# Kernel optimization log

Hardware: AMD Instinct MI355X
Metric: run time of the kernel (lower is better)

## Reference

```python
import jax, jax.numpy as jnp
import numpy as np

B = 8
A = 1614
TOPN = 6
IOU_THR = 0.25
PAD = 224
OUT = 224

def _make_anchors():
    # 6 anchor shapes on the 14x14 map, 6 on 7x7, 9 on 4x4 -> 1614 total,
    # ordered anchor-type-major then row-major spatial to match the [C,H,W] flatten
    # of the tidy conv outputs (as generate_default_anchor_maps does in NTS-Net).
    specs = [
        (14, 32.0, [(48, 48), (64, 48), (48, 64), (80, 80), (96, 64), (64, 96)]),
        (7, 64.0, [(96, 96), (128, 96), (96, 128), (160, 160), (192, 128), (128, 192)]),
        (4, 112.0, [(192, 192), (256, 192), (192, 256), (288, 288), (320, 256), (256, 320), (352, 352), (384, 320), (320, 384)]),
    ]
    blocks = []
    for fm, stride, sizes in specs:
        c = (np.arange(fm) + 0.5) * stride
        cy, cx = np.meshgrid(c, c, indexing='ij')
        for (h, w) in sizes:
            blocks.append(np.stack([cy - h / 2, cx - w / 2, cy + h / 2, cx + w / 2], -1).reshape(-1, 4))
    a = (np.concatenate(blocks, 0) + PAD).astype(np.int64)  # mimic (edge_anchors+224).astype(int)
    return a.astype(np.float32)  # [1614,4] (y0,x0,y1,x1) in padded-image coords

def _conv(x, w, b, stride, pad):
    y = jax.lax.conv_general_dilated(x, w, (stride, stride), [(pad, pad), (pad, pad)],
                                     dimension_numbers=('NCHW', 'OIHW', 'NCHW'))
    return y + b[None, :, None, None]

def _rpn_scores(rpn, wd1, bd1, wd2, bd2, wd3, bd3, wt1, bt1, wt2, bt2, wt3, bt3):
    b = rpn.shape[0]
    d1 = jax.nn.relu(_conv(rpn, wd1, bd1, 1, 1))   # [B,128,14,14]
    d2 = jax.nn.relu(_conv(d1, wd2, bd2, 2, 1))    # [B,128,7,7]
    d3 = jax.nn.relu(_conv(d2, wd3, bd3, 2, 1))    # [B,128,4,4]
    t1 = _conv(d1, wt1, bt1, 1, 0).reshape(b, -1)  # [B,1176]
    t2 = _conv(d2, wt2, bt2, 1, 0).reshape(b, -1)  # [B,294]
    t3 = _conv(d3, wt3, bt3, 1, 0).reshape(b, -1)  # [B,144]
    return jnp.concatenate([t1, t2, t3], axis=1)   # [B,1614]

def _nms_keep(boxes, scores):
    # Greedy NMS over all A anchors; returns keep mask in ORIGINAL anchor order.
    order = jnp.argsort(-scores)
    b = boxes[order]
    y0, x0, y1, x1 = b[:, 0], b[:, 1], b[:, 2], b[:, 3]
    area = (y1 - y0) * (x1 - x0)
    ih = jnp.clip(jnp.minimum(y1[:, None], y1[None, :]) - jnp.maximum(y0[:, None], y0[None, :]), 0)
    iw = jnp.clip(jnp.minimum(x1[:, None], x1[None, :]) - jnp.maximum(x0[:, None], x0[None, :]), 0)
    inter = ih * iw
    iou = inter / (area[:, None] + area[None, :] - inter)
    idx = jnp.arange(A)
    def body(i, supp):
        row = (iou[i] > IOU_THR) & (idx > i)
        return jnp.where(supp[i], supp, supp | row)
    supp = jax.lax.fori_loop(0, A, body, jnp.zeros((A,), bool))
    return jnp.zeros((A,), bool).at[order].set(~supp)

def _crop_resize(img, box):
    # img [3,Hp,Wp]; box int32 (x0,y0,x1,y1).
    # Equivalent to F.interpolate(img[:, y0:y1, x0:x1], (224,224), 'bilinear', align_corners=True)
    x0, y0, x1, y1 = box[0], box[1], box[2], box[3]
    t = jnp.arange(OUT, dtype=jnp.float32) / (OUT - 1)
    sy = y0.astype(jnp.float32) + t * (y1 - 1 - y0).astype(jnp.float32)
    sx = x0.astype(jnp.float32) + t * (x1 - 1 - x0).astype(jnp.float32)
    y0i = jnp.floor(sy).astype(jnp.int32); x0i = jnp.floor(sx).astype(jnp.int32)
    y1i = jnp.minimum(y0i + 1, y1 - 1);    x1i = jnp.minimum(x0i + 1, x1 - 1)
    wy = (sy - y0i.astype(jnp.float32))[None, :, None]
    wx = (sx - x0i.astype(jnp.float32))[None, None, :]
    g = lambda yi, xi: img[:, yi][:, :, xi]  # gather rows then cols -> [3,224,224]
    top = (1 - wx) * g(y0i, x0i) + wx * g(y0i, x1i)
    bot = (1 - wx) * g(y1i, x0i) + wx * g(y1i, x1i)
    return (1 - wy) * top + wy * bot

def setup_inputs():
    key = jax.random.key(0)
    ks = jax.random.split(key, 16)
    n = jax.random.normal
    return {
        'x': n(ks[0], (B, 3, 448, 448), jnp.float32),
        'rpn_feature': n(ks[1], (B, 2048, 14, 14), jnp.float32),
        'anchors': jnp.asarray(_make_anchors()),
        'wd1': 0.02 * n(ks[2], (128, 2048, 3, 3), jnp.float32), 'bd1': 0.01 * n(ks[3], (128,), jnp.float32),
        'wd2': 0.05 * n(ks[4], (128, 128, 3, 3), jnp.float32),  'bd2': 0.01 * n(ks[5], (128,), jnp.float32),
        'wd3': 0.05 * n(ks[6], (128, 128, 3, 3), jnp.float32),  'bd3': 0.01 * n(ks[7], (128,), jnp.float32),
        'wt1': 0.1 * n(ks[8], (6, 128, 1, 1), jnp.float32),     'bt1': 0.01 * n(ks[9], (6,), jnp.float32),
        'wt2': 0.1 * n(ks[10], (6, 128, 1, 1), jnp.float32),    'bt2': 0.01 * n(ks[11], (6,), jnp.float32),
        'wt3': 0.1 * n(ks[12], (9, 128, 1, 1), jnp.float32),    'bt3': 0.01 * n(ks[13], (9,), jnp.float32),
    }

def reference(x, rpn_feature, anchors, wd1, bd1, wd2, bd2, wd3, bd3, wt1, bt1, wt2, bt2, wt3, bt3):
    scores = _rpn_scores(rpn_feature, wd1, bd1, wd2, bd2, wd3, bd3, wt1, bt1, wt2, bt2, wt3, bt3)
    keep = jax.vmap(lambda s: _nms_keep(anchors, s))(scores)           # [B,A] bool
    masked = jnp.where(keep, scores, -jnp.inf)
    top_prob, top_idx = jax.lax.top_k(masked, TOPN)                    # [B,6]
    tb = anchors[top_idx]                                              # [B,6,4] (y0,x0,y1,x1)
    coords = jnp.stack([tb[..., 1], tb[..., 0], tb[..., 3], tb[..., 2]], -1)  # (x0,y0,x1,y1)
    x_pad = jnp.pad(x, ((0, 0), (0, 0), (PAD, PAD), (PAD, PAD)))       # [B,3,896,896]
    bint = coords.astype(jnp.int32)
    part_imgs = jax.vmap(lambda img, bs: jax.vmap(lambda bb: _crop_resize(img, bb))(bs))(x_pad, bint)  # [B,6,3,224,224]
    return part_imgs, coords, top_prob, top_idx
```

## Files before the change

kernel.cpp:

```cpp
#include <hip/hip_runtime.h>
#include <hip/hip_bf16.h>
#include <math.h>
#include <stdint.h>


#define OFF_COORDS 7225344
#define OFF_PROB   7225536
#define OFF_IDX    7225584
#define NA 1614
#define K1TOT 18432

typedef __attribute__((ext_vector_type(8)))  short  short8;
typedef __attribute__((ext_vector_type(16))) float  floatx16;

__global__ __launch_bounds__(256) void k_prep_all(
    const float* __restrict__ rpn,
    const float* __restrict__ wd1,
    const float* __restrict__ wd2,
    const float* __restrict__ wd3,
    __hip_bfloat16* __restrict__ ah,  __hip_bfloat16* __restrict__ al,
    __hip_bfloat16* __restrict__ b1h, __hip_bfloat16* __restrict__ b1l,
    __hip_bfloat16* __restrict__ b2h, __hip_bfloat16* __restrict__ b2l,
    __hip_bfloat16* __restrict__ b3h, __hip_bfloat16* __restrict__ b3l)
{
    const int bid = blockIdx.x;
    const int t   = threadIdx.x;
    if (bid < 1024) {
        __shared__ float tile[64][65];
        const int cib  = (bid & 31) * 64;
        const int posb = ((bid >> 5) & 3) * 64;
        const int b    = bid >> 7;
#pragma unroll
        for (int it = 0; it < 16; ++it) {
            int idx  = it * 256 + t;
            int cil  = idx >> 6;
            int posl = idx & 63;
            int pos  = posb + posl;
            int py = pos >> 4, px = pos & 15;
            int y = py - 1, x = px - 1;
            float v = 0.0f;
            if ((unsigned)y < 14u && (unsigned)x < 14u)
                v = rpn[((size_t)(b * 2048 + cib + cil) * 14 + y) * 14 + x];
            tile[cil][posl] = v;
        }
        __syncthreads();
#pragma unroll
        for (int it = 0; it < 16; ++it) {
            int idx  = it * 256 + t;
            int posl = idx >> 6;
            int cil  = idx & 63;
            float v = tile[cil][posl];
            __hip_bfloat16 h = __float2bfloat16(v);
            __hip_bfloat16 l = __float2bfloat16(v - __bfloat162float(h));
            size_t o = (size_t)(b * 256 + posb + posl) * 2048 + cib + cil;
            ah[o] = h; al[o] = l;
        }
    } else if (bid < 2176) {
        int local = bid - 1024;
        int tap = local % 9;
        int co  = local / 9;
#pragma unroll
        for (int i = 0; i < 8; ++i) {
            int ci = i * 256 + t;
            float v = wd1[((size_t)co * 2048 + ci) * 9 + tap];
            __hip_bfloat16 h = __float2bfloat16(v);
            __hip_bfloat16 l = __float2bfloat16(v - __bfloat162float(h));
            size_t o = (size_t)co * K1TOT + tap * 2048 + ci;
            b1h[o] = h; b1l[o] = l;
        }
    } else {
        int local = bid - 2176;
        int z  = local >= 576;
        int l3 = z ? (local - 576) : local;
        int tap = l3 % 9;
        int co  = (l3 / 9) * 2 + (t >> 7);
        int ci  = t & 127;
        const float* w = z ? wd3 : wd2;
        __hip_bfloat16* bh = z ? b3h : b2h;
        __hip_bfloat16* bl = z ? b3l : b2l;
        float v = w[((size_t)co * 128 + ci) * 9 + tap];
        __hip_bfloat16 h = __float2bfloat16(v);
        __hip_bfloat16 l = __float2bfloat16(v - __bfloat162float(h));
        size_t o = (size_t)co * 1152 + tap * 128 + ci;
        bh[o] = h; bl[o] = l;
    }
}

template<int POSN, int OW, int STR, int CIN, int MTOT, bool SWIZ>
__global__ __launch_bounds__(256) void k_conv_mfma(const short* __restrict__ ah,
                                                   const short* __restrict__ al,
                                                   const short* __restrict__ bh,
                                                   const short* __restrict__ bl,
                                                   float* __restrict__ partial,
                                                   int chunk, int kpx, int mtiles)
{
    constexpr int KTOT = CIN * 9;
    __shared__ short AsH[128][40];
    __shared__ short AsL[128][40];
    __shared__ short BsH[128][40];
    __shared__ short BsL[128][40];

    int mt, kc;
    if (SWIZ) {
        int bid = blockIdx.x;
        int xcd = bid & 7;
        int idx = bid >> 3;
        int q   = idx / mtiles;
        kc = xcd * kpx + q;
        mt = idx - q * mtiles;
    } else {
        mt = blockIdx.x;
        kc = blockIdx.y;
    }

    const int t     = threadIdx.x;
    const int lane  = t & 63;
    const int w     = t >> 6;
    const int wm    = (w & 1) * 64;
    const int wn    = (w >> 1) * 64;
    const int lm    = lane & 31;
    const int half  = lane >> 5;
    const int mbase = mt * 128;
    const int k0    = kc * chunk;
    const int k1    = (k0 + chunk < KTOT) ? (k0 + chunk) : KTOT;

    int arow[2], apos[2]; bool aval[2];
    const int akc = (t & 3) * 8;
#pragma unroll
    for (int i = 0; i < 2; ++i) {
        int row = ((i * 256 + t) >> 2);
        int m   = mbase + row;
        arow[i] = row;
        aval[i] = (m < MTOT);
        int mm = aval[i] ? m : 0;
        int b  = mm / POSN;
        int p  = mm - b * POSN;
        int y  = p / OW;
        int x  = p - y * OW;
        apos[i] = b * 256 + y * STR * 16 + x * STR;
    }

    floatx16 acc[2][2];
#pragma unroll
    for (int mf = 0; mf < 2; ++mf)
#pragma unroll
        for (int nf = 0; nf < 2; ++nf)
#pragma unroll
            for (int r = 0; r < 16; ++r) acc[mf][nf][r] = 0.0f;

    const short8 zero8 = {0, 0, 0, 0, 0, 0, 0, 0};

    for (int ks = k0; ks < k1; ks += 32) {
        const int tap = ks / CIN;
        const int ci0 = ks - tap * CIN;
        const int dy  = tap / 3, dx = tap - dy * 3;
#pragma unroll
        for (int i = 0; i < 2; ++i) {
            short8 vh = zero8, vl = zero8;
            if (aval[i]) {
                size_t g = (size_t)(apos[i] + dy * 16 + dx) * CIN + ci0 + akc;
                vh = *(const short8*)(ah + g);
                vl = *(const short8*)(al + g);
            }
            *(short8*)&AsH[arow[i]][akc] = vh;
            *(short8*)&AsL[arow[i]][akc] = vl;
        }
#pragma unroll
        for (int i = 0; i < 2; ++i) {
            int n = ((i * 256 + t) >> 2);
            size_t g = (size_t)n * KTOT + ks + akc;
            *(short8*)&BsH[n][akc] = *(const short8*)(bh + g);
            *(short8*)&BsL[n][akc] = *(const short8*)(bl + g);
        }
        __syncthreads();
#pragma unroll
        for (int kst = 0; kst < 2; ++kst) {
            const int koff = kst * 16 + half * 8;
            short8 a_h[2], a_l[2], b_h[2], b_l[2];
#pragma unroll
            for (int mf = 0; mf < 2; ++mf) {
                a_h[mf] = *(const short8*)&AsH[wm + mf * 32 + lm][koff];
                a_l[mf] = *(const short8*)&AsL[wm + mf * 32 + lm][koff];
            }
#pragma unroll
            for (int nf = 0; nf < 2; ++nf) {
                b_h[nf] = *(const short8*)&BsH[wn + nf * 32 + lm][koff];
                b_l[nf] = *(const short8*)&BsL[wn + nf * 32 + lm][koff];
            }
#pragma unroll
            for (int mf = 0; mf < 2; ++mf)
#pragma unroll
                for (int nf = 0; nf < 2; ++nf) {
                    acc[mf][nf] = __builtin_amdgcn_mfma_f32_32x32x16_bf16(
                        a_h[mf], b_h[nf], acc[mf][nf], 0, 0, 0);
                    acc[mf][nf] = __builtin_amdgcn_mfma_f32_32x32x16_bf16(
                        a_h[mf], b_l[nf], acc[mf][nf], 0, 0, 0);
                    acc[mf][nf] = __builtin_amdgcn_mfma_f32_32x32x16_bf16(
                        a_l[mf], b_h[nf], acc[mf][nf], 0, 0, 0);
                }
        }
        __syncthreads();
    }

    float* P = partial + (size_t)kc * MTOT * 128;
#pragma unroll
    for (int mf = 0; mf < 2; ++mf)
#pragma unroll
        for (int nf = 0; nf < 2; ++nf)
#pragma unroll
            for (int r = 0; r < 16; ++r) {
                int row = (r & 3) + 8 * (r >> 2) + 4 * half;
                int m = mbase + wm + mf * 32 + row;
                int n = wn + nf * 32 + lm;
                if (m < MTOT) P[(size_t)m * 128 + n] = acc[mf][nf][r];
            }
}

template<int POSN, int OWV>
__global__ __launch_bounds__(256) void k_reduce_pad(const float* __restrict__ partial,
                                                    const float* __restrict__ bias,
                                                    float* __restrict__ dn,
                                                    __hip_bfloat16* __restrict__ ph,
                                                    __hip_bfloat16* __restrict__ pl,
                                                    int S)
{
    constexpr int MTOT = 8 * POSN;
    int idx = blockIdx.x * 256 + threadIdx.x;
    int b   = idx >> 15;
    int pos = (idx >> 7) & 255;
    int co  = idx & 127;
    int y = (pos >> 4) - 1;
    int x = (pos & 15) - 1;
    if ((unsigned)y < (unsigned)OWV && (unsigned)x < (unsigned)OWV) {
        int m = b * POSN + y * OWV + x;
        float s = bias[co];
        for (int k = 0; k < S; ++k) s += partial[(size_t)k * MTOT * 128 + m * 128 + co];
        s = fmaxf(s, 0.0f);
        dn[(size_t)m * 128 + co] = s;
        __hip_bfloat16 h = __float2bfloat16(s);
        __hip_bfloat16 l = __float2bfloat16(s - __bfloat162float(h));
        ph[idx] = h; pl[idx] = l;
    } else {
        ph[idx] = __float2bfloat16(0.0f);
        pl[idx] = __float2bfloat16(0.0f);
    }
}

__global__ __launch_bounds__(256) void k_reduce3(const float* __restrict__ partial,
                                                 const float* __restrict__ bias,
                                                 float* __restrict__ dn, int S)
{
    int idx = blockIdx.x * 256 + threadIdx.x;
    int co  = idx & 127;
    float s = bias[co];
    for (int k = 0; k < S; ++k) s += partial[(size_t)k * 128 * 128 + idx];
    dn[idx] = fmaxf(s, 0.0f);
}

__global__ __launch_bounds__(256) void k_heads(const float* __restrict__ d1n,
                                               const float* __restrict__ d2n,
                                               const float* __restrict__ d3n,
                                               const float* __restrict__ w1, const float* __restrict__ b1,
                                               const float* __restrict__ w2, const float* __restrict__ b2,
                                               const float* __restrict__ w3, const float* __restrict__ b3,
                                               float* __restrict__ scores)
{
    int idx = blockIdx.x * 256 + threadIdx.x;
    if (idx >= 8 * NA) return;
    int b = idx / NA;
    int e = idx - b * NA;
    const float* d; const float* w; float bias;
    if (e < 1176) {
        int c = e / 196, p = e - c * 196;
        d = d1n + (size_t)(b * 196 + p) * 128; w = w1 + c * 128; bias = b1[c];
    } else if (e < 1470) {
        int e2 = e - 1176; int c = e2 / 49, p = e2 - c * 49;
        d = d2n + (size_t)(b * 49 + p) * 128; w = w2 + c * 128; bias = b2[c];
    } else {
        int e2 = e - 1470; int c = e2 / 16, p = e2 - c * 16;
        d = d3n + (size_t)(b * 16 + p) * 128; w = w3 + c * 128; bias = b3[c];
    }
    float s = bias;
#pragma unroll
    for (int i = 0; i < 32; ++i) {
        float4 dv = ((const float4*)d)[i];
        float4 wv = ((const float4*)w)[i];
        s = fmaf(dv.x, wv.x, s);
        s = fmaf(dv.y, wv.y, s);
        s = fmaf(dv.z, wv.z, s);
        s = fmaf(dv.w, wv.w, s);
    }
    scores[idx] = s;
}

__global__ __launch_bounds__(256) void k_nms_topk(const float* __restrict__ scores,
                                                  const float* __restrict__ anchors,
                                                  float* __restrict__ out,
                                                  int* __restrict__ boxes)
{
    __shared__ float ms[NA];
    __shared__ float ay0[NA], ax0[NA], ay1[NA], ax1[NA];
    __shared__ unsigned char picked[NA];
    __shared__ float rv[4]; __shared__ int ri[4];
    __shared__ float win[5];
    int b = blockIdx.x;
    int t = threadIdx.x;
    for (int i = t; i < NA; i += 256) {
        ms[i] = scores[b * NA + i];
        float4 an = ((const float4*)anchors)[i];
        ay0[i] = an.x; ax0[i] = an.y; ay1[i] = an.z; ax1[i] = an.w;
        picked[i] = 0;
    }
    __syncthreads();
    for (int r = 0; r < 6; ++r) {
        float bv = -INFINITY; int bi = NA;
        for (int i = t; i < NA; i += 256) {
            if (!picked[i]) {
                float v = ms[i];
                if (v > bv || (v == bv && i < bi)) { bv = v; bi = i; }
            }
        }
#pragma unroll
        for (int off = 32; off > 0; off >>= 1) {
            float v2 = __shfl_down(bv, off);
            int   i2 = __shfl_down(bi, off);
            if (v2 > bv || (v2 == bv && i2 < bi)) { bv = v2; bi = i2; }
        }
        if ((t & 63) == 0) { rv[t >> 6] = bv; ri[t >> 6] = bi; }
        __syncthreads();
        if (t == 0) {
            bv = rv[0]; bi = ri[0];
            for (int wv = 1; wv < 4; ++wv)
                if (rv[wv] > bv || (rv[wv] == bv && ri[wv] < bi)) { bv = rv[wv]; bi = ri[wv]; }
            picked[bi] = 1;
            win[0] = ay0[bi]; win[1] = ax0[bi]; win[2] = ay1[bi]; win[3] = ax1[bi]; win[4] = bv;
            int o = b * 6 + r;
            out[OFF_COORDS + o * 4 + 0] = ax0[bi];
            out[OFF_COORDS + o * 4 + 1] = ay0[bi];
            out[OFF_COORDS + o * 4 + 2] = ax1[bi];
            out[OFF_COORDS + o * 4 + 3] = ay1[bi];
            out[OFF_PROB + o] = bv;
            out[OFF_IDX  + o] = (float)bi;
            boxes[o * 4 + 0] = (int)ax0[bi];
            boxes[o * 4 + 1] = (int)ay0[bi];
            boxes[o * 4 + 2] = (int)ax1[bi];
            boxes[o * 4 + 3] = (int)ay1[bi];
        }
        __syncthreads();
        float by0 = win[0], bx0 = win[1], by1 = win[2], bx1 = win[3];
        float barea = (by1 - by0) * (bx1 - bx0);
        for (int i = t; i < NA; i += 256) {
            if (picked[i]) continue;
            float ih = fmaxf(fminf(by1, ay1[i]) - fmaxf(by0, ay0[i]), 0.0f);
            float iw = fmaxf(fminf(bx1, ax1[i]) - fmaxf(bx0, ax0[i]), 0.0f);
            float inter = ih * iw;
            float area  = (ay1[i] - ay0[i]) * (ax1[i] - ax0[i]);
            float iou = inter / (barea + area - inter);
            if (iou > 0.25f) ms[i] = -INFINITY;
        }
        __syncthreads();
    }
}

__global__ __launch_bounds__(256) void k_crop(const float* __restrict__ x,
                                              const int* __restrict__ boxes,
                                              float* __restrict__ out)
{
    int lin = blockIdx.x * 256 + threadIdx.x;
    int i    = lin % 224;
    int rest = lin / 224;
    int j    = rest % 224;
    int rc   = rest / 224;
    int c    = rc % 3;
    int br   = rc / 3;
    int b    = br / 6;
    int4 bx = ((const int4*)boxes)[br];
    float tj = (float)j / 223.0f;
    float sy = (float)bx.y + tj * (float)(bx.w - 1 - bx.y);
    int y0i = (int)floorf(sy);
    int y1i = min(y0i + 1, bx.w - 1);
    float wy = sy - (float)y0i;
    float ti = (float)i / 223.0f;
    float sx = (float)bx.x + ti * (float)(bx.z - 1 - bx.x);
    int x0i = (int)floorf(sx);
    int x1i = min(x0i + 1, bx.z - 1);
    float wx = sx - (float)x0i;
    const float* img = x + ((size_t)b * 3 + c) * 448 * 448;
    auto g = [&](int yy, int xx) -> float {
        yy -= 224; xx -= 224;
        if ((unsigned)yy >= 448u || (unsigned)xx >= 448u) return 0.0f;
        return img[(size_t)yy * 448 + xx];
    };
    float g00 = g(y0i, x0i), g01 = g(y0i, x1i);
    float g10 = g(y1i, x0i), g11 = g(y1i, x1i);
    float top = (1.0f - wx) * g00 + wx * g01;
    float bot = (1.0f - wx) * g10 + wx * g11;
    out[lin] = (1.0f - wy) * top + wy * bot;
}

extern "C" void kernel_launch(void* const* d_in, const int* in_sizes, int n_in,
                              void* d_out, int out_size, void* d_ws, size_t ws_size,
                              hipStream_t stream)
{
    (void)in_sizes; (void)n_in; (void)out_size;
    const float* x    = (const float*)d_in[0];
    const float* rpn  = (const float*)d_in[1];
    const float* anch = (const float*)d_in[2];
    const float* wd1  = (const float*)d_in[3];
    const float* bd1  = (const float*)d_in[4];
    const float* wd2  = (const float*)d_in[5];
    const float* bd2  = (const float*)d_in[6];
    const float* wd3  = (const float*)d_in[7];
    const float* bd3  = (const float*)d_in[8];
    const float* hw1  = (const float*)d_in[9];
    const float* hb1  = (const float*)d_in[10];
    const float* hw2  = (const float*)d_in[11];
    const float* hb2  = (const float*)d_in[12];
    const float* hw3  = (const float*)d_in[13];
    const float* hb3  = (const float*)d_in[14];
    float* out = (float*)d_out;

    char* ws = (char*)d_ws;
    size_t off = 0;
    auto alloc = [&](size_t bytes) -> void* {
        void* p = ws + off;
        off = (off + bytes + 255) & ~(size_t)255;
        return p;
    };
    __hip_bfloat16* ahb  = (__hip_bfloat16*)alloc((size_t)8 * 256 * 2048 * 2);
    __hip_bfloat16* alb  = (__hip_bfloat16*)alloc((size_t)8 * 256 * 2048 * 2);
    __hip_bfloat16* b1h  = (__hip_bfloat16*)alloc((size_t)128 * K1TOT * 2);
    __hip_bfloat16* b1l  = (__hip_bfloat16*)alloc((size_t)128 * K1TOT * 2);
    __hip_bfloat16* b2h  = (__hip_bfloat16*)alloc((size_t)128 * 1152 * 2);
    __hip_bfloat16* b2l  = (__hip_bfloat16*)alloc((size_t)128 * 1152 * 2);
    __hip_bfloat16* b3h  = (__hip_bfloat16*)alloc((size_t)128 * 1152 * 2);
    __hip_bfloat16* b3l  = (__hip_bfloat16*)alloc((size_t)128 * 1152 * 2);
    __hip_bfloat16* d1ph = (__hip_bfloat16*)alloc((size_t)8 * 256 * 128 * 2);
    __hip_bfloat16* d1pl = (__hip_bfloat16*)alloc((size_t)8 * 256 * 128 * 2);
    __hip_bfloat16* d2ph = (__hip_bfloat16*)alloc((size_t)8 * 256 * 128 * 2);
    __hip_bfloat16* d2pl = (__hip_bfloat16*)alloc((size_t)8 * 256 * 128 * 2);
    float* d1n  = (float*)alloc((size_t)8 * 196 * 128 * 4);
    float* d2n  = (float*)alloc((size_t)8 * 49 * 128 * 4);
    float* d3n  = (float*)alloc((size_t)8 * 16 * 128 * 4);
    float* sc   = (float*)alloc((size_t)8 * NA * 4);
    int*  boxes = (int*)alloc((size_t)8 * 6 * 4 * 4);
    size_t avail = (ws_size > off) ? (ws_size - off) : 0;
    float* P = (float*)(ws + off);

    int S1 = (avail >= (size_t)64 * 1568 * 128 * 4) ? 64 : 48;
    if (avail < (size_t)48 * 1568 * 128 * 4) S1 = 32;
    int chunk1 = K1TOT / S1;
    int kpx1   = S1 / 8;

    k_prep_all<<<dim3(3328), 256, 0, stream>>>(rpn, wd1, wd2, wd3,
        ahb, alb, b1h, b1l, b2h, b2l, b3h, b3l);

    k_conv_mfma<196, 14, 1, 2048, 1568, true><<<dim3(13 * S1), 256, 0, stream>>>(
        (const short*)ahb, (const short*)alb, (const short*)b1h, (const short*)b1l,
        P, chunk1, kpx1, 13);
    k_reduce_pad<196, 14><<<dim3(1024), 256, 0, stream>>>(P, bd1, d1n, d1ph, d1pl, S1);

    k_conv_mfma<49, 7, 2, 128, 392, false><<<dim3(4, 9), 256, 0, stream>>>(
        (const short*)d1ph, (const short*)d1pl, (const short*)b2h, (const short*)b2l,
        P, 128, 0, 0);
    k_reduce_pad<49, 7><<<dim3(1024), 256, 0, stream>>>(P, bd2, d2n, d2ph, d2pl, 9);

    k_conv_mfma<16, 4, 2, 128, 128, false><<<dim3(1, 9), 256, 0, stream>>>(
        (const short*)d2ph, (const short*)d2pl, (const short*)b3h, (const short*)b3l,
        P, 128, 0, 0);
    k_reduce3<<<dim3(64), 256, 0, stream>>>(P, bd3, d3n, 9);

    k_heads<<<dim3((8 * NA + 255) / 256), 256, 0, stream>>>(d1n, d2n, d3n,
        hw1, hb1, hw2, hb2, hw3, hb3, sc);
    k_nms_topk<<<dim3(8), 256, 0, stream>>>(sc, anch, out, boxes);
    k_crop<<<dim3(28224), 256, 0, stream>>>(x, boxes, out);
}
```

Baseline: 268.6 us.

## Fuse conv2/conv3 reductions and heads into producers, add register-prefetch pipeline

```diff
diff --git a/kernel.cpp b/kernel.cpp
--- a/kernel.cpp
+++ b/kernel.cpp
@@ -21,7 +21,8 @@
     __hip_bfloat16* __restrict__ ah,  __hip_bfloat16* __restrict__ al,
     __hip_bfloat16* __restrict__ b1h, __hip_bfloat16* __restrict__ b1l,
     __hip_bfloat16* __restrict__ b2h, __hip_bfloat16* __restrict__ b2l,
-    __hip_bfloat16* __restrict__ b3h, __hip_bfloat16* __restrict__ b3l)
+    __hip_bfloat16* __restrict__ b3h, __hip_bfloat16* __restrict__ b3l,
+    __hip_bfloat16* __restrict__ d2ph, __hip_bfloat16* __restrict__ d2pl)
 {
     const int bid = blockIdx.x;
     const int t   = threadIdx.x;
@@ -68,7 +69,7 @@
             size_t o = (size_t)co * K1TOT + tap * 2048 + ci;
             b1h[o] = h; b1l[o] = l;
         }
-    } else {
+    } else if (bid < 3328) {
         int local = bid - 2176;
         int z  = local >= 576;
         int l3 = z ? (local - 576) : local;
@@ -83,35 +84,27 @@
         __hip_bfloat16 l = __float2bfloat16(v - __bfloat162float(h));
         size_t o = (size_t)co * 1152 + tap * 128 + ci;
         bh[o] = h; bl[o] = l;
-    }
-}
-
-template<int POSN, int OW, int STR, int CIN, int MTOT, bool SWIZ>
-__global__ __launch_bounds__(256) void k_conv_mfma(const short* __restrict__ ah,
-                                                   const short* __restrict__ al,
-                                                   const short* __restrict__ bh,
-                                                   const short* __restrict__ bl,
-                                                   float* __restrict__ partial,
-                                                   int chunk, int kpx, int mtiles)
+    } else {
+        const short8 z8 = {0,0,0,0,0,0,0,0};
+        int idx = (bid - 3328) * 256 + t;
+        if (idx < 32768) ((short8*)d2ph)[idx] = z8;
+        else             ((short8*)d2pl)[idx - 32768] = z8;
+    }
+}
+
+template<int POSN, int OW, int STR, int CIN, int MTOT, int EPI>
+__global__ __launch_bounds__(256) void k_conv_mfma(
+    const short* __restrict__ ah, const short* __restrict__ al,
+    const short* __restrict__ bh, const short* __restrict__ bl,
+    float* __restrict__ fout,
+    __hip_bfloat16* __restrict__ ph, __hip_bfloat16* __restrict__ pl,
+    const float* __restrict__ bias, int chunk)
 {
     constexpr int KTOT = CIN * 9;
     __shared__ short AsH[128][40];
     __shared__ short AsL[128][40];
     __shared__ short BsH[128][40];
     __shared__ short BsL[128][40];
-
-    int mt, kc;
-    if (SWIZ) {
-        int bid = blockIdx.x;
-        int xcd = bid & 7;
-        int idx = bid >> 3;
-        int q   = idx / mtiles;
-        kc = xcd * kpx + q;
-        mt = idx - q * mtiles;
-    } else {
-        mt = blockIdx.x;
-        kc = blockIdx.y;
-    }
 
     const int t     = threadIdx.x;
     const int lane  = t & 63;
@@ -120,6 +113,8 @@
     const int wn    = (w >> 1) * 64;
     const int lm    = lane & 31;
     const int half  = lane >> 5;
+    const int mt    = blockIdx.x;
+    const int kc    = blockIdx.y;
     const int mbase = mt * 128;
     const int k0    = kc * chunk;
     const int k1    = (k0 + chunk < KTOT) ? (k0 + chunk) : KTOT;
@@ -149,30 +144,39 @@
             for (int r = 0; r < 16; ++r) acc[mf][nf][r] = 0.0f;
 
     const short8 zero8 = {0, 0, 0, 0, 0, 0, 0, 0};
-
-    for (int ks = k0; ks < k1; ks += 32) {
+    short8 rAh[2], rAl[2], rBh[2], rBl[2];
+
+    auto load_stage = [&](int ks) {
         const int tap = ks / CIN;
         const int ci0 = ks - tap * CIN;
         const int dy  = tap / 3, dx = tap - dy * 3;
 #pragma unroll
         for (int i = 0; i < 2; ++i) {
-            short8 vh = zero8, vl = zero8;
             if (aval[i]) {
                 size_t g = (size_t)(apos[i] + dy * 16 + dx) * CIN + ci0 + akc;
-                vh = *(const short8*)(ah + g);
-                vl = *(const short8*)(al + g);
-            }
-            *(short8*)&AsH[arow[i]][akc] = vh;
-            *(short8*)&AsL[arow[i]][akc] = vl;
+                rAh[i] = *(const short8*)(ah + g);
+                rAl[i] = *(const short8*)(al + g);
+            } else { rAh[i] = zero8; rAl[i] = zero8; }
         }
 #pragma unroll
         for (int i = 0; i < 2; ++i) {
             int n = ((i * 256 + t) >> 2);
             size_t g = (size_t)n * KTOT + ks + akc;
-            *(short8*)&BsH[n][akc] = *(const short8*)(bh + g);
-            *(short8*)&BsL[n][akc] = *(const short8*)(bl + g);
-        }
-        __syncthreads();
+            rBh[i] = *(const short8*)(bh + g);
+            rBl[i] = *(const short8*)(bl + g);
+        }
+    };
+    auto store_stage = [&]() {
+#pragma unroll
+        for (int i = 0; i < 2; ++i) {
+            *(short8*)&AsH[arow[i]][akc] = rAh[i];
+            *(short8*)&AsL[arow[i]][akc] = rAl[i];
+            int n = ((i * 256 + t) >> 2);
+            *(short8*)&BsH[n][akc] = rBh[i];
+            *(short8*)&BsL[n][akc] = rBl[i];
+        }
+    };
+    auto compute = [&]() {
 #pragma unroll
         for (int kst = 0; kst < 2; ++kst) {
             const int koff = kst * 16 + half * 8;
@@ -199,21 +203,57 @@
                         a_l[mf], b_h[nf], acc[mf][nf], 0, 0, 0);
                 }
         }
-        __syncthreads();
-    }
-
-    float* P = partial + (size_t)kc * MTOT * 128;
-#pragma unroll
-    for (int mf = 0; mf < 2; ++mf)
-#pragma unroll
-        for (int nf = 0; nf < 2; ++nf)
-#pragma unroll
-            for (int r = 0; r < 16; ++r) {
-                int row = (r & 3) + 8 * (r >> 2) + 4 * half;
-                int m = mbase + wm + mf * 32 + row;
-                int n = wn + nf * 32 + lm;
-                if (m < MTOT) P[(size_t)m * 128 + n] = acc[mf][nf][r];
-            }
+    };
+
+    load_stage(k0);
+    store_stage();
+    for (int ks = k0 + 32; ks < k1; ks += 32) {
+        __syncthreads();
+        load_stage(ks);
+        compute();
+        __syncthreads();
+        store_stage();
+    }
+    __syncthreads();
+    compute();
+
+    if constexpr (EPI == 0) {
+        float* P = fout + (size_t)kc * MTOT * 128;
+#pragma unroll
+        for (int mf = 0; mf < 2; ++mf)
+#pragma unroll
+            for (int nf = 0; nf < 2; ++nf)
+#pragma unroll
+                for (int r = 0; r < 16; ++r) {
+                    int row = (r & 3) + 8 * (r >> 2) + 4 * half;
+                    int m = mbase + wm + mf * 32 + row;
+                    int n = wn + nf * 32 + lm;
+                    if (m < MTOT) P[(size_t)m * 128 + n] = acc[mf][nf][r];
+                }
+    } else {
+#pragma unroll
+        for (int mf = 0; mf < 2; ++mf)
+#pragma unroll
+            for (int nf = 0; nf < 2; ++nf)
+#pragma unroll
+                for (int r = 0; r < 16; ++r) {
+                    int row = (r & 3) + 8 * (r >> 2) + 4 * half;
+                    int m = mbase + wm + mf * 32 + row;
+                    int n = wn + nf * 32 + lm;
+                    if (m < MTOT) {
+                        float s = fmaxf(acc[mf][nf][r] + bias[n], 0.0f);
+                        fout[(size_t)m * 128 + n] = s;
+                        if constexpr (EPI == 1) {
+                            int b = m / POSN, p = m - b * POSN;
+                            int y = p / OW,   x = p - y * OW;
+                            int o = (b * 256 + (y + 1) * 16 + (x + 1)) * 128 + n;
+                            __hip_bfloat16 h = __float2bfloat16(s);
+                            ph[o] = h;
+                            pl[o] = __float2bfloat16(s - __bfloat162float(h));
+                        }
+                    }
+                }
+    }
 }
 
 template<int POSN, int OWV>
@@ -246,57 +286,14 @@
     }
 }
 
-__global__ __launch_bounds__(256) void k_reduce3(const float* __restrict__ partial,
-                                                 const float* __restrict__ bias,
-                                                 float* __restrict__ dn, int S)
-{
-    int idx = blockIdx.x * 256 + threadIdx.x;
-    int co  = idx & 127;
-    float s = bias[co];
-    for (int k = 0; k < S; ++k) s += partial[(size_t)k * 128 * 128 + idx];
-    dn[idx] = fmaxf(s, 0.0f);
-}
-
-__global__ __launch_bounds__(256) void k_heads(const float* __restrict__ d1n,
-                                               const float* __restrict__ d2n,
-                                               const float* __restrict__ d3n,
-                                               const float* __restrict__ w1, const float* __restrict__ b1,
-                                               const float* __restrict__ w2, const float* __restrict__ b2,
-                                               const float* __restrict__ w3, const float* __restrict__ b3,
-                                               float* __restrict__ scores)
-{
-    int idx = blockIdx.x * 256 + threadIdx.x;
-    if (idx >= 8 * NA) return;
-    int b = idx / NA;
-    int e = idx - b * NA;
-    const float* d; const float* w; float bias;
-    if (e < 1176) {
-        int c = e / 196, p = e - c * 196;
-        d = d1n + (size_t)(b * 196 + p) * 128; w = w1 + c * 128; bias = b1[c];
-    } else if (e < 1470) {
-        int e2 = e - 1176; int c = e2 / 49, p = e2 - c * 49;
-        d = d2n + (size_t)(b * 49 + p) * 128; w = w2 + c * 128; bias = b2[c];
-    } else {
-        int e2 = e - 1470; int c = e2 / 16, p = e2 - c * 16;
-        d = d3n + (size_t)(b * 16 + p) * 128; w = w3 + c * 128; bias = b3[c];
-    }
-    float s = bias;
-#pragma unroll
-    for (int i = 0; i < 32; ++i) {
-        float4 dv = ((const float4*)d)[i];
-        float4 wv = ((const float4*)w)[i];
-        s = fmaf(dv.x, wv.x, s);
-        s = fmaf(dv.y, wv.y, s);
-        s = fmaf(dv.z, wv.z, s);
-        s = fmaf(dv.w, wv.w, s);
-    }
-    scores[idx] = s;
-}
-
-__global__ __launch_bounds__(256) void k_nms_topk(const float* __restrict__ scores,
-                                                  const float* __restrict__ anchors,
-                                                  float* __restrict__ out,
-                                                  int* __restrict__ boxes)
+__global__ __launch_bounds__(256) void k_nms_topk(
+    const float* __restrict__ d1n, const float* __restrict__ d2n,
+    const float* __restrict__ d3n,
+    const float* __restrict__ w1, const float* __restrict__ b1,
+    const float* __restrict__ w2, const float* __restrict__ b2,
+    const float* __restrict__ w3, const float* __restrict__ b3,
+    const float* __restrict__ anchors,
+    float* __restrict__ out, int* __restrict__ boxes)
 {
     __shared__ float ms[NA];
     __shared__ float ay0[NA], ax0[NA], ay1[NA], ax1[NA];
@@ -305,8 +302,31 @@
     __shared__ float win[5];
     int b = blockIdx.x;
     int t = threadIdx.x;
+    for (int e = t; e < NA; e += 256) {
+        const float* d; const float* w; float bias;
+        if (e < 1176) {
+            int c = e / 196, p = e - c * 196;
+            d = d1n + (size_t)(b * 196 + p) * 128; w = w1 + c * 128; bias = b1[c];
+        } else if (e < 1470) {
+            int e2 = e - 1176; int c = e2 / 49, p = e2 - c * 49;
+            d = d2n + (size_t)(b * 49 + p) * 128; w = w2 + c * 128; bias = b2[c];
+        } else {
+            int e2 = e - 1470; int c = e2 / 16, p = e2 - c * 16;
+            d = d3n + (size_t)(b * 16 + p) * 128; w = w3 + c * 128; bias = b3[c];
+        }
+        float s = bias;
+#pragma unroll
+        for (int i = 0; i < 32; ++i) {
+            float4 dv = ((const float4*)d)[i];
+            float4 wv = ((const float4*)w)[i];
+            s = fmaf(dv.x, wv.x, s);
+            s = fmaf(dv.y, wv.y, s);
+            s = fmaf(dv.z, wv.z, s);
+            s = fmaf(dv.w, wv.w, s);
+        }
+        ms[e] = s;
+    }
     for (int i = t; i < NA; i += 256) {
-        ms[i] = scores[b * NA + i];
         float4 an = ((const float4*)anchors)[i];
         ay0[i] = an.x; ax0[i] = an.y; ay1[i] = an.z; ax1[i] = an.w;
         picked[i] = 0;
@@ -442,36 +462,33 @@
     float* d1n  = (float*)alloc((size_t)8 * 196 * 128 * 4);
     float* d2n  = (float*)alloc((size_t)8 * 49 * 128 * 4);
     float* d3n  = (float*)alloc((size_t)8 * 16 * 128 * 4);
-    float* sc   = (float*)alloc((size_t)8 * NA * 4);
     int*  boxes = (int*)alloc((size_t)8 * 6 * 4 * 4);
     size_t avail = (ws_size > off) ? (ws_size - off) : 0;
     float* P = (float*)(ws + off);
 
-    int S1 = (avail >= (size_t)64 * 1568 * 128 * 4) ? 64 : 48;
+    int S1 = 48;
     if (avail < (size_t)48 * 1568 * 128 * 4) S1 = 32;
+    if (avail < (size_t)32 * 1568 * 128 * 4) S1 = 16;
     int chunk1 = K1TOT / S1;
-    int kpx1   = S1 / 8;
-
-    k_prep_all<<<dim3(3328), 256, 0, stream>>>(rpn, wd1, wd2, wd3,
-        ahb, alb, b1h, b1l, b2h, b2l, b3h, b3l);
-
-    k_conv_mfma<196, 14, 1, 2048, 1568, true><<<dim3(13 * S1), 256, 0, stream>>>(
+
+    k_prep_all<<<dim3(3584), 256, 0, stream>>>(rpn, wd1, wd2, wd3,
+        ahb, alb, b1h, b1l, b2h, b2l, b3h, b3l, d2ph, d2pl);
+
+    k_conv_mfma<196, 14, 1, 2048, 1568, 0><<<dim3(13, S1), 256, 0, stream>>>(
         (const short*)ahb, (const short*)alb, (const short*)b1h, (const short*)b1l,
-        P, chunk1, kpx1, 13);
+        P, nullptr, nullptr, nullptr, chunk1);
     k_reduce_pad<196, 14><<<dim3(1024), 256, 0, stream>>>(P, bd1, d1n, d1ph, d1pl, S1);
 
-    k_conv_mfma<49, 7, 2, 128, 392, false><<<dim3(4, 9), 256, 0, stream>>>(
+    k_conv_mfma<49, 7, 2, 128, 392, 1><<<dim3(4, 1), 256, 0, stream>>>(
         (const short*)d1ph, (const short*)d1pl, (const short*)b2h, (const short*)b2l,
-        P, 128, 0, 0);
-    k_reduce_pad<49, 7><<<dim3(1024), 256, 0, stream>>>(P, bd2, d2n, d2ph, d2pl, 9);
-
-    k_conv_mfma<16, 4, 2, 128, 128, false><<<dim3(1, 9), 256, 0, stream>>>(
+        d2n, d2ph, d2pl, bd2, 1152);
+
+    k_conv_mfma<16, 4, 2, 128, 128, 2><<<dim3(1, 1), 256, 0, stream>>>(
         (const short*)d2ph, (const short*)d2pl, (const short*)b3h, (const short*)b3l,
-        P, 128, 0, 0);
-    k_reduce3<<<dim3(64), 256, 0, stream>>>(P, bd3, d3n, 9);
-
-    k_heads<<<dim3((8 * NA + 255) / 256), 256, 0, stream>>>(d1n, d2n, d3n,
-        hw1, hb1, hw2, hb2, hw3, hb3, sc);
-    k_nms_topk<<<dim3(8), 256, 0, stream>>>(sc, anch, out, boxes);
+        d3n, nullptr, nullptr, bd3, 1152);
+
+    k_nms_topk<<<dim3(8), 256, 0, stream>>>(d1n, d2n, d3n,
+        hw1, hb1, hw2, hb2, hw3, hb3, anch, out, boxes);
+
     k_crop<<<dim3(28224), 256, 0, stream>>>(x, boxes, out);
 }
```

After: 347.8 us. 1.29x slower.
